# Kernel optimization log

Measured on AMD Instinct MI355X. Metric: run time of the kernel, lower is better.

## Reference

```python
import jax, jax.numpy as jnp
import numpy as np

COUPLE_STRENGTH = 0.1
ITER_FISTA = 16
ITER_EIGENVAL = 20


def setup_inputs() -> dict:
    key = jax.random.key(0)
    k1, k2 = jax.random.split(key)
    # light field patches: (b, N, u, v, s, t, ch)
    x = jax.random.normal(k1, (8, 256, 5, 5, 4, 4, 3), dtype=jnp.float32)
    dim_signal = 5 * 5 * 4 * 4 * 3  # 1200
    dim_dict = 2 * dim_signal       # overcompleteness = 2 -> 2400
    D = jax.random.normal(k2, (dim_signal, dim_dict), dtype=jnp.float32)
    D = D / jnp.linalg.norm(D, axis=0, keepdims=True)  # UnitNorm(axis=0) constraint
    return {"x": x, "dictionary": D}


def _max_eigval(D):
    """von Mises power iteration for largest eigenvalue of D^T D."""
    v0 = jax.random.normal(jax.random.key(42), (D.shape[1],), dtype=D.dtype)
    v0 = v0 / jnp.linalg.norm(v0)

    def step(v, _):
        w = D.T @ (D @ v)
        n = jnp.linalg.norm(w)
        return w / n, n

    _, norms = jax.lax.scan(step, v0, None, length=ITER_EIGENVAL)
    return norms[-1]


def _soft_threshold(x, thr):
    return jnp.sign(x) * jnp.maximum(jnp.abs(x) - thr, 0.0)


def _sparse_code_fista(x2, D):
    """x2: (B, N, dim_signal); D: (dim_signal, dim_dict) -> codes (B, N, dim_dict)."""
    L = _max_eigval(D)            # Lipschitz constant of grad of 0.5*||Dz - x||^2
    thr = COUPLE_STRENGTH / L
    z0 = jnp.zeros(x2.shape[:-1] + (D.shape[1],), dtype=x2.dtype)
    carry0 = (z0, z0, jnp.float32(1.0))  # (z, y, t)

    def step(carry, _):
        z, y, t = carry
        recon = jnp.einsum('bnk,dk->bnd', y, D)             # (B,N,ds)
        grad = jnp.einsum('bnd,dk->bnk', recon - x2, D)     # (B,N,dd)
        z_new = _soft_threshold(y - grad / L, thr)
        t_new = 0.5 * (1.0 + jnp.sqrt(1.0 + 4.0 * t * t))
        y_new = z_new + ((t - 1.0) / t_new) * (z_new - z)   # Nesterov momentum
        return (z_new, y_new, t_new), None

    (z, _, _), _ = jax.lax.scan(step, carry0, None, length=ITER_FISTA)
    return z


def reference(x, dictionary):
    B, N, u, v, s, t, ch = x.shape
    x2 = x.reshape(B, N, u * v * s * t * ch)
    code = jax.lax.stop_gradient(_sparse_code_fista(x2, dictionary))
    recon = jnp.einsum('bnk,dk->bnd', code, dictionary)  # matmul(x, D, transpose_b=True)
    return recon.reshape(B, N, u, v, s, t, ch)
```

## Files before the change

### kernel.cpp

```cpp
#include <hip/hip_runtime.h>
#include <hip/hip_bf16.h>
#include <cmath>

#define DS 1200
#define DD 2400
#define MR 2048
#define KP 1216
#define NP1 1280
#define NG 2432
#define PPI 150

typedef __attribute__((ext_vector_type(8))) short s16x8;
typedef __attribute__((ext_vector_type(4))) float f32x4;

__device__ __forceinline__ float s2f(short s) {
    union { unsigned u; float f; } c;
    c.u = ((unsigned)(unsigned short)s) << 16;
    return c.f;
}
__device__ __forceinline__ short f2s(float f) {
    __hip_bfloat16 h = __float2bfloat16(f);
    return *reinterpret_cast<short*>(&h);
}


__device__ __forceinline__ unsigned rotl32(unsigned x, int d) {
    return (x << d) | (x >> (32 - d));
}

__device__ void threefry2x32(unsigned k0, unsigned k1, unsigned x0, unsigned x1,
                             unsigned* o0, unsigned* o1) {
    unsigned ks0 = k0, ks1 = k1, ks2 = k0 ^ k1 ^ 0x1BD11BDAu;
    const int rotA[4] = {13, 15, 26, 6};
    const int rotB[4] = {17, 29, 16, 24};
    x0 += ks0; x1 += ks1;
    #pragma unroll
    for (int r = 0; r < 4; r++) { x0 += x1; x1 = rotl32(x1, rotA[r]); x1 ^= x0; }
    x0 += ks1; x1 += ks2 + 1u;
    #pragma unroll
    for (int r = 0; r < 4; r++) { x0 += x1; x1 = rotl32(x1, rotB[r]); x1 ^= x0; }
    x0 += ks2; x1 += ks0 + 2u;
    #pragma unroll
    for (int r = 0; r < 4; r++) { x0 += x1; x1 = rotl32(x1, rotA[r]); x1 ^= x0; }
    x0 += ks0; x1 += ks1 + 3u;
    #pragma unroll
    for (int r = 0; r < 4; r++) { x0 += x1; x1 = rotl32(x1, rotB[r]); x1 ^= x0; }
    x0 += ks1; x1 += ks2 + 4u;
    #pragma unroll
    for (int r = 0; r < 4; r++) { x0 += x1; x1 = rotl32(x1, rotA[r]); x1 ^= x0; }
    x0 += ks2; x1 += ks0 + 5u;
    *o0 = x0; *o1 = x1;
}

__device__ float erfinv_f32(float x) {
    float w = -logf((1.0f - x) * (1.0f + x));
    float p;
    if (w < 5.0f) {
        w -= 2.5f;
        p = 2.81022636e-08f;
        p = fmaf(p, w, 3.43273939e-07f);
        p = fmaf(p, w, -3.5233877e-06f);
        p = fmaf(p, w, -4.39150654e-06f);
        p = fmaf(p, w, 0.00021858087f);
        p = fmaf(p, w, -0.00125372503f);
        p = fmaf(p, w, -0.00417768164f);
        p = fmaf(p, w, 0.246640727f);
        p = fmaf(p, w, 1.50140941f);
    } else {
        w = sqrtf(w) - 3.0f;
        p = -0.000200214257f;
        p = fmaf(p, w, 0.000100950558f);
        p = fmaf(p, w, 0.00134934322f);
        p = fmaf(p, w, -0.00367342844f);
        p = fmaf(p, w, 0.00573950773f);
        p = fmaf(p, w, -0.0076224613f);
        p = fmaf(p, w, 0.00943887047f);
        p = fmaf(p, w, 1.00167406f);
        p = fmaf(p, w, 2.83297682f);
    }
    return p * x;
}

__device__ float bits_to_normal(unsigned bits) {
    unsigned fb = (bits >> 9) | 0x3F800000u;
    float u01 = __uint_as_float(fb) - 1.0f;
    const float lo = -0.99999994f;
    float u = u01 * 2.0f + lo;
    u = fmaxf(lo, u);
    return 1.41421356237f * erfinv_f32(u);
}

__global__ void k_init(float* __restrict__ w0, float* __restrict__ w1,
                       float* __restrict__ part) {
    int tid = threadIdx.x;
    for (int i = tid; i < 21 * PPI; i += 256) part[i] = 0.0f;
    if (tid < 32) {
        w0[2400 + tid] = 0.0f;
        w1[2400 + tid] = 0.0f;
    }
    __shared__ float red[256];
    float local2 = 0.0f;
    for (int p = tid; p < DS; p += 256) {
        unsigned r0, r1;
        threefry2x32(0u, 42u, (unsigned)p, (unsigned)(DS + p), &r0, &r1);
        float n0 = bits_to_normal(r0);
        float n1 = bits_to_normal(r1);
        w0[p] = n0;
        w0[DS + p] = n1;
        local2 += n0 * n0 + n1 * n1;
    }
    red[tid] = local2;
    __syncthreads();
    for (int s = 128; s > 0; s >>= 1) {
        if (tid < s) red[tid] += red[tid + s];
        __syncthreads();
    }
    if (tid == 0) part[0] = red[0];
}

__global__ __launch_bounds__(1024) void k_gmv(const short* __restrict__ Grm,
                                              const float* __restrict__ win,
                                              const float* __restrict__ partin,
                                              float* __restrict__ wout,
                                              float* __restrict__ partout) {
    float s2 = 0.0f;
    for (int i = 0; i < PPI; i++) s2 += partin[i];
    float rn = 1.0f / sqrtf(s2);
    int wave = threadIdx.x >> 6, lane = threadIdx.x & 63;
    int row = blockIdx.x * 16 + wave;
    const s16x8* gh = (const s16x8*)(Grm + (size_t)row * NG);
    const float4* w4 = (const float4*)win;
    float acc = 0.0f;
    #pragma unroll
    for (int i = 0; i < 5; i++) {
        int c = lane + i * 64;
        if (c < 304) {
            s16x8 h = gh[c];
            float4 wa = w4[c * 2], wb = w4[c * 2 + 1];
            acc += s2f(h[0]) * wa.x + s2f(h[1]) * wa.y;
            acc += s2f(h[2]) * wa.z + s2f(h[3]) * wa.w;
            acc += s2f(h[4]) * wb.x + s2f(h[5]) * wb.y;
            acc += s2f(h[6]) * wb.z + s2f(h[7]) * wb.w;
        }
    }
    #pragma unroll
    for (int off = 32; off > 0; off >>= 1) acc += __shfl_xor(acc, off, 64);
    __shared__ float red[16];
    if (lane == 0) {
        float val = acc * rn;
        wout[row] = val;
        red[wave] = val * val;
    }
    __syncthreads();
    if (threadIdx.x == 0) {
        float s = 0.0f;
        #pragma unroll
        for (int i = 0; i < 16; i++) s += red[i];
        partout[blockIdx.x] = s;
    }
}

__global__ void k_fin(const float* __restrict__ part20, float* __restrict__ scal) {
    if (threadIdx.x == 0) {
        float s = 0.0f;
        for (int i = 0; i < PPI; i++) s += part20[i];
        float L = sqrtf(s);
        scal[0] = L;
        scal[1] = 1.0f / L;
        scal[2] = 0.1f / L;
    }
}

__global__ void k_makeD(const float* __restrict__ D, short* __restrict__ Dp) {
    int p = blockIdx.x * 256 + threadIdx.x;
    if (p >= NP1 * NG) return;
    int tile = p >> 10, win = p & 1023;
    int row = win >> 3, e = win & 7;
    int mt = tile / (NG >> 3), ct = tile % (NG >> 3);
    int d = mt * 128 + row, n = ct * 8 + e;
    float v = (d < DS && n < DD) ? D[(size_t)d * DD + n] : 0.0f;
    Dp[p] = f2s(v);
}

__global__ void k_makeX(const float* __restrict__ x,
                        short* __restrict__ Xhi, short* __restrict__ Xlo) {
    int p = blockIdx.x * 256 + threadIdx.x;
    if (p >= MR * KP) return;
    int tile = p >> 10, win = p & 1023;
    int row = win >> 3, e = win & 7;
    int mt = tile / (KP >> 3), ct = tile % (KP >> 3);
    int m = mt * 128 + row, k = ct * 8 + e;
    float v = (k < DS) ? x[(size_t)m * DS + k] : 0.0f;
    short h = f2s(v);
    Xhi[p] = h;
    Xlo[p] = f2s(v - s2f(h));
}

__global__ void k_makeDt(const float* __restrict__ D,
                         short* __restrict__ Dthi, short* __restrict__ Dtlo) {
    __shared__ float t[32][33];
    int bc = blockIdx.x * 32;
    int bk = blockIdx.y * 32;
    int tx = threadIdx.x & 31, ty = threadIdx.x >> 5;
    for (int i = ty; i < 32; i += 8) {
        int k = bk + i, c = bc + tx;
        t[i][tx] = (k < DS && c < DD) ? D[(size_t)k * DD + c] : 0.0f;
    }
    __syncthreads();
    for (int i = ty; i < 32; i += 8) {
        int c = bc + i, k = bk + tx;
        float v = t[tx][i];
        short h = f2s(v);
        size_t po = ((size_t)(c >> 7) * (KP >> 3) + (k >> 3)) * 1024 +
                    ((c & 127) << 3) + (k & 7);
        Dthi[po] = h;
        Dtlo[po] = f2s(v - s2f(h));
    }
}

__global__ void k_fista0(const float* __restrict__ XD, const float* __restrict__ scal,
                         short* __restrict__ Z, short* __restrict__ Y) {
    int i = blockIdx.x * 256 + threadIdx.x;
    if (i >= MR * NG / 8) return;
    float invL = scal[1], thr = scal[2];
    int e0 = i * 8;
    int band = e0 / (128 * NG);
    int rem = e0 - band * (128 * NG);
    int tile = rem >> 10;
    int row = (rem & 1023) >> 3;
    int m = band * 128 + row;
    int n = tile * 8;
    const float4* xp = (const float4*)(XD + (size_t)m * NG + n);
    float4 v0 = xp[0], v1 = xp[1];
    float vs[8] = {v0.x, v0.y, v0.z, v0.w, v1.x, v1.y, v1.z, v1.w};
    s16x8 zs;
    #pragma unroll
    for (int k = 0; k < 8; k++) {
        float gs = vs[k] * invL;
        float az = fabsf(gs) - thr;
        float zn = (az > 0.0f) ? copysignf(az, gs) : 0.0f;
        zs[k] = f2s(zn);
    }
    ((s16x8*)Z)[i] = zs;
    ((s16x8*)Y)[i] = zs;
}

__device__ __forceinline__ void gload16(const void* g, void* l) {
    __builtin_amdgcn_global_load_lds(
        (const __attribute__((address_space(1))) unsigned int*)g,
        (__attribute__((address_space(3))) unsigned int*)l, 16, 0, 0);
}

template <int EPI, bool SPLIT>
__global__ __launch_bounds__(256, 4) void mfma_gemm(
    const short* __restrict__ Ah, const short* __restrict__ Al, int CA,
    const short* __restrict__ Bh, const short* __restrict__ Bl, int CB,
    int K, int swz,
    const float* __restrict__ XDc, const float* __restrict__ scal, float mom,
    short* __restrict__ Ynew, short* __restrict__ Zst,
    short* __restrict__ Gp, short* __restrict__ Grm,
    float* __restrict__ Out) {
    constexpr int ALO = 2048;
    constexpr int BHO = SPLIT ? 4096 : 2048;
    constexpr int BLO = 8192;
    constexpr int BUF = SPLIT ? 12288 : 6144;
    __shared__ __align__(16) short lds[2 * BUF];

    const int tid = threadIdx.x;
    const int w = tid >> 6, lane = tid & 63;
    const int fm = lane & 15, kg = lane >> 4;
    const int wr = w >> 1, wc = w & 1;

    int bx, by;
    if (swz) {
        int q = gridDim.x >> 3;
        int s = (blockIdx.x & 7) * q + (blockIdx.x >> 3);
        by = s & 31; bx = s >> 5;
    } else { bx = blockIdx.x; by = blockIdx.y; }
    const int m0 = by * 64, n0 = bx * 128;

    f32x4 acc[2][4];
    #pragma unroll
    for (int g = 0; g < 2; ++g)
        #pragma unroll
        for (int h = 0; h < 4; ++h) acc[g][h] = f32x4{0.f, 0.f, 0.f, 0.f};

    float invL = 0.0f, thr = 0.0f;
    if (EPI == 2) { invL = scal[1]; thr = scal[2]; }

    const int half = (m0 >> 6) & 1;
    const size_t Aoff = (size_t)(m0 & ~127) * CA + w * 1024 + half * 512 + lane * 8;
    const size_t Boff = (size_t)n0 * CB + w * 512 + lane * 8;

    const int nk = K >> 5;

    auto STAGE = [&](int t, int cur) {
        const int kk = t << 12;
        short* bp = &lds[cur * BUF];
        gload16(Ah + Aoff + kk, bp + w * 512);
        gload16(Bh + Boff + kk, bp + BHO + w * 512);
        gload16(Bh + Boff + kk + 2048, bp + BHO + 2048 + w * 512);
        if constexpr (SPLIT) {
            gload16(Al + Aoff + kk, bp + ALO + w * 512);
            gload16(Bl + Boff + kk, bp + BLO + w * 512);
            gload16(Bl + Boff + kk + 2048, bp + BLO + 2048 + w * 512);
        }
    };

    STAGE(0, 0);

    for (int t = 0; t < nk; ++t) {
        __syncthreads();
        if (t + 1 < nk) STAGE(t + 1, (t + 1) & 1);
        const short* bs = &lds[(t & 1) * BUF];

        s16x8 a[2], b[4];
        #pragma unroll
        for (int g = 0; g < 2; ++g)
            a[g] = *(const s16x8*)&bs[kg * 512 + (wr * 32 + g * 16 + fm) * 8];
        #pragma unroll
        for (int h = 0; h < 4; ++h)
            b[h] = *(const s16x8*)&bs[BHO + kg * 1024 + (wc * 64 + h * 16 + fm) * 8];
        if constexpr (SPLIT) {
            s16x8 a2[2], b2[4];
            #pragma unroll
            for (int g = 0; g < 2; ++g)
                a2[g] = *(const s16x8*)&bs[ALO + kg * 512 + (wr * 32 + g * 16 + fm) * 8];
            #pragma unroll
            for (int h = 0; h < 4; ++h)
                b2[h] = *(const s16x8*)&bs[BLO + kg * 1024 + (wc * 64 + h * 16 + fm) * 8];
            #pragma unroll
            for (int g = 0; g < 2; ++g)
                #pragma unroll
                for (int h = 0; h < 4; ++h) {
                    acc[g][h] = __builtin_amdgcn_mfma_f32_16x16x32_bf16(a[g], b[h], acc[g][h], 0, 0, 0);
                    acc[g][h] = __builtin_amdgcn_mfma_f32_16x16x32_bf16(a[g], b2[h], acc[g][h], 0, 0, 0);
                    acc[g][h] = __builtin_amdgcn_mfma_f32_16x16x32_bf16(a2[g], b[h], acc[g][h], 0, 0, 0);
                }
        } else {
            #pragma unroll
            for (int g = 0; g < 2; ++g)
                #pragma unroll
                for (int h = 0; h < 4; ++h)
                    acc[g][h] = __builtin_amdgcn_mfma_f32_16x16x32_bf16(a[g], b[h], acc[g][h], 0, 0, 0);
        }
    }

    #pragma unroll
    for (int g = 0; g < 2; ++g) {
        #pragma unroll
        for (int h = 0; h < 4; ++h) {
            #pragma unroll
            for (int j = 0; j < 4; ++j) {
                int m = m0 + wr * 32 + g * 16 + kg * 4 + j;
                int n = n0 + wc * 64 + h * 16 + fm;
                float v = acc[g][h][j];
                if (EPI == 0) {
                    if (n < DS) Out[(size_t)m * DS + n] = v;
                } else if (EPI == 2) {
                    size_t o = (size_t)m * NG + n;
                    size_t pz = (size_t)(m & ~127) * NG + ((n >> 3) << 10) +
                                ((m & 127) << 3) + (n & 7);
                    float grad = v - XDc[o];
                    float yold = s2f(Ah[pz]);
                    float zold = s2f(Zst[pz]);
                    float gs = yold - grad * invL;
                    float az = fabsf(gs) - thr;
                    float zn = (az > 0.0f) ? copysignf(az, gs) : 0.0f;
                    float yn = zn + mom * (zn - zold);
                    Zst[pz] = f2s(zn);
                    Ynew[pz] = f2s(yn);
                } else if (EPI == 3) {
                    Out[(size_t)m * NG + n] = v;
                } else {
                    size_t pz = (size_t)(m & ~127) * NG + ((n >> 3) << 10) +
                                ((m & 127) << 3) + (n & 7);
                    short hv = f2s(v);
                    Gp[pz] = hv;
                    Grm[(size_t)m * NG + n] = hv;
                }
            }
        }
    }
}

extern "C" void kernel_launch(void* const* d_in, const int* in_sizes, int n_in,
                              void* d_out, int out_size, void* d_ws, size_t ws_size,
                              hipStream_t stream) {
    const float* x = (const float*)d_in[0];
    const float* D = (const float*)d_in[1];
    float* out = (float*)d_out;

    char* wsb = (char*)d_ws;
    float* w0 = (float*)wsb;
    float* w1 = w0 + 2432;
    float* part = w1 + 2432;
    float* scal = part + 3200;

    char* p = wsb + 65536;
    short* Dp   = (short*)p; p += (size_t)NP1 * NG * 2;
    short* Dthi = (short*)p; p += (size_t)NG * KP * 2;
    short* Dtlo = (short*)p; p += (size_t)NG * KP * 2;
    short* Xhi  = (short*)p; p += (size_t)MR * KP * 2;
    short* Xlo  = (short*)p; p += (size_t)MR * KP * 2;
    short* Gp   = (short*)p; p += (size_t)NG * NG * 2;
    short* Grm  = (short*)p; p += (size_t)NG * NG * 2;
    float* XD   = (float*)p; p += (size_t)MR * NG * 4;
    short* Ya   = (short*)p; p += (size_t)MR * NG * 2;
    short* Yb   = (short*)p; p += (size_t)MR * NG * 2;
    short* Zp   = (short*)p; p += (size_t)MR * NG * 2;

    k_makeD<<<(NP1 * NG + 255) / 256, 256, 0, stream>>>(D, Dp);
    k_makeDt<<<dim3(NG / 32, KP / 32), 256, 0, stream>>>(D, Dthi, Dtlo);
    k_makeX<<<(MR * KP + 255) / 256, 256, 0, stream>>>(x, Xhi, Xlo);

    mfma_gemm<4, true><<<dim3(NG / 128, NG / 64), 256, 0, stream>>>(
        Dthi, Dtlo, KP, Dthi, Dtlo, KP, KP, 0,
        nullptr, nullptr, 0.0f, nullptr, nullptr, Gp, Grm, nullptr);

    mfma_gemm<3, true><<<dim3(608), 256, 0, stream>>>(
        Xhi, Xlo, KP, Dthi, Dtlo, KP, KP, 1,
        nullptr, nullptr, 0.0f, nullptr, nullptr, nullptr, nullptr, XD);

    k_init<<<1, 256, 0, stream>>>(w0, w1, part);
    for (int j = 0; j < 20; j++) {
        const float* win = (j & 1) ? w1 : w0;
        float* wout = (j & 1) ? w0 : w1;
        k_gmv<<<PPI, 1024, 0, stream>>>(Grm, win, part + j * PPI, wout,
                                        part + (j + 1) * PPI);
    }
    k_fin<<<1, 64, 0, stream>>>(part + 20 * PPI, scal);

    k_fista0<<<(MR * NG / 8 + 255) / 256, 256, 0, stream>>>(XD, scal, Zp, Ya);

    float t = 1.6180339887f;
    for (int i = 1; i < 16; i++) {
        float tn = 0.5f * (1.0f + sqrtf(1.0f + 4.0f * t * t));
        float mom = (t - 1.0f) / tn;
        t = tn;
        short* Yc = (i & 1) ? Ya : Yb;
        short* Yn = (i & 1) ? Yb : Ya;
        mfma_gemm<2, false><<<dim3(608), 256, 0, stream>>>(
            Yc, nullptr, NG, Gp, nullptr, NG, NG, 1,
            XD, scal, mom, Yn, Zp, nullptr, nullptr, nullptr);
    }

    mfma_gemm<0, false><<<dim3(320), 256, 0, stream>>>(
        Zp, nullptr, NG, Dp, nullptr, NG, NG, 1,
        nullptr, nullptr, 0.0f, nullptr, nullptr, nullptr, nullptr, out);
}
```

Measured before the change: 940.5 us.

## Fold identity and step size into Gram matrix; deepen K per stage in FISTA GEMM

Builds W = I - G/L in bf16 once after the power iteration, so each FISTA step computes y·W directly and the epilogue becomes a single fma with XD·invL instead of reading the old Y and subtracting. The non-split GEMM path now stages 64-wide K slices per barrier, two MFMA sub-steps per stage, halving the number of syncs and loop iterations. It adds an fp32 Gram buffer (aliased onto Ya) and a conversion kernel, and puts the identity-plus-scaled-Gram values into bf16, which may change rounding.

```diff
diff --git a/kernel.cpp b/kernel.cpp
--- a/kernel.cpp
+++ b/kernel.cpp
@@ -218,6 +218,30 @@
     }
 }
 
+__global__ void k_makeW(const float* __restrict__ Gf, const float* __restrict__ scal,
+                        short* __restrict__ Wp) {
+    int i = blockIdx.x * 256 + threadIdx.x;
+    if (i >= NG * NG / 8) return;
+    float invL = scal[1];
+    int e0 = i * 8;
+    int band = e0 / (128 * NG);
+    int rem = e0 - band * (128 * NG);
+    int tile = rem >> 10;
+    int row = (rem & 1023) >> 3;
+    int m = band * 128 + row;
+    int k0 = tile * 8;
+    const float4* gp = (const float4*)(Gf + (size_t)m * NG + k0);
+    float4 g0 = gp[0], g1 = gp[1];
+    float gv[8] = {g0.x, g0.y, g0.z, g0.w, g1.x, g1.y, g1.z, g1.w};
+    s16x8 wv;
+    #pragma unroll
+    for (int e = 0; e < 8; e++) {
+        float wf = ((k0 + e == m) ? 1.0f : 0.0f) - gv[e] * invL;
+        wv[e] = f2s(wf);
+    }
+    ((s16x8*)Wp)[i] = wv;
+}
+
 __global__ void k_fista0(const float* __restrict__ XD, const float* __restrict__ scal,
                          short* __restrict__ Z, short* __restrict__ Y) {
     int i = blockIdx.x * 256 + threadIdx.x;
@@ -258,12 +282,12 @@
     int K, int swz,
     const float* __restrict__ XDc, const float* __restrict__ scal, float mom,
     short* __restrict__ Ynew, short* __restrict__ Zst,
-    short* __restrict__ Gp, short* __restrict__ Grm,
+    short* __restrict__ Grm,
     float* __restrict__ Out) {
     constexpr int ALO = 2048;
-    constexpr int BHO = SPLIT ? 4096 : 2048;
+    constexpr int BHO = 4096;
     constexpr int BLO = 8192;
-    constexpr int BUF = SPLIT ? 12288 : 6144;
+    constexpr int BUF = 12288;
     __shared__ __align__(16) short lds[2 * BUF];
 
     const int tid = threadIdx.x;
@@ -289,21 +313,32 @@
     if (EPI == 2) { invL = scal[1]; thr = scal[2]; }
 
     const int half = (m0 >> 6) & 1;
-    const size_t Aoff = (size_t)(m0 & ~127) * CA + w * 1024 + half * 512 + lane * 8;
-    const size_t Boff = (size_t)n0 * CB + w * 512 + lane * 8;
-
-    const int nk = K >> 5;
+    const int nk = K / (SPLIT ? 32 : 64);
+
+    const size_t AbS = (size_t)(m0 & ~127) * CA + w * 1024 + half * 512 + lane * 8;
+    const size_t BbS = (size_t)n0 * CB + w * 512 + lane * 8;
+    const size_t AbN = (size_t)(m0 & ~127) * CA + half * 512 + lane * 8;
+    const size_t BbN = (size_t)n0 * CB + lane * 8;
 
     auto STAGE = [&](int t, int cur) {
-        const int kk = t << 12;
         short* bp = &lds[cur * BUF];
-        gload16(Ah + Aoff + kk, bp + w * 512);
-        gload16(Bh + Boff + kk, bp + BHO + w * 512);
-        gload16(Bh + Boff + kk + 2048, bp + BHO + 2048 + w * 512);
         if constexpr (SPLIT) {
-            gload16(Al + Aoff + kk, bp + ALO + w * 512);
-            gload16(Bl + Boff + kk, bp + BLO + w * 512);
-            gload16(Bl + Boff + kk + 2048, bp + BLO + 2048 + w * 512);
+            const size_t kk = (size_t)t << 12;
+            gload16(Ah + AbS + kk, bp + w * 512);
+            gload16(Bh + BbS + kk, bp + BHO + w * 512);
+            gload16(Bh + BbS + kk + 2048, bp + BHO + 2048 + w * 512);
+            gload16(Al + AbS + kk, bp + ALO + w * 512);
+            gload16(Bl + BbS + kk, bp + BLO + w * 512);
+            gload16(Bl + BbS + kk + 2048, bp + BLO + 2048 + w * 512);
+        } else {
+            const size_t kk = (size_t)t << 13;
+            const int cs0 = 2 * w, cs1 = 2 * w + 1;
+            gload16(Ah + AbN + kk + cs0 * 1024, bp + cs0 * 512);
+            gload16(Ah + AbN + kk + cs1 * 1024, bp + cs1 * 512);
+            gload16(Bh + BbN + kk + cs0 * 1024,       bp + BHO + cs0 * 1024);
+            gload16(Bh + BbN + kk + cs0 * 1024 + 512, bp + BHO + cs0 * 1024 + 512);
+            gload16(Bh + BbN + kk + cs1 * 1024,       bp + BHO + cs1 * 1024);
+            gload16(Bh + BbN + kk + cs1 * 1024 + 512, bp + BHO + cs1 * 1024 + 512);
         }
     };
 
@@ -314,35 +349,39 @@
         if (t + 1 < nk) STAGE(t + 1, (t + 1) & 1);
         const short* bs = &lds[(t & 1) * BUF];
 
-        s16x8 a[2], b[4];
         #pragma unroll
-        for (int g = 0; g < 2; ++g)
-            a[g] = *(const s16x8*)&bs[kg * 512 + (wr * 32 + g * 16 + fm) * 8];
-        #pragma unroll
-        for (int h = 0; h < 4; ++h)
-            b[h] = *(const s16x8*)&bs[BHO + kg * 1024 + (wc * 64 + h * 16 + fm) * 8];
-        if constexpr (SPLIT) {
-            s16x8 a2[2], b2[4];
+        for (int ks = 0; ks < (SPLIT ? 1 : 2); ++ks) {
+            const int c = ks * 4 + kg;
+            s16x8 a[2], b[4];
             #pragma unroll
             for (int g = 0; g < 2; ++g)
-                a2[g] = *(const s16x8*)&bs[ALO + kg * 512 + (wr * 32 + g * 16 + fm) * 8];
+                a[g] = *(const s16x8*)&bs[c * 512 + (wr * 32 + g * 16 + fm) * 8];
             #pragma unroll
             for (int h = 0; h < 4; ++h)
-                b2[h] = *(const s16x8*)&bs[BLO + kg * 1024 + (wc * 64 + h * 16 + fm) * 8];
-            #pragma unroll
-            for (int g = 0; g < 2; ++g)
+                b[h] = *(const s16x8*)&bs[BHO + c * 1024 + (wc * 64 + h * 16 + fm) * 8];
+            if constexpr (SPLIT) {
+                s16x8 a2[2], b2[4];
                 #pragma unroll
-                for (int h = 0; h < 4; ++h) {
-                    acc[g][h] = __builtin_amdgcn_mfma_f32_16x16x32_bf16(a[g], b[h], acc[g][h], 0, 0, 0);
-                    acc[g][h] = __builtin_amdgcn_mfma_f32_16x16x32_bf16(a[g], b2[h], acc[g][h], 0, 0, 0);
-                    acc[g][h] = __builtin_amdgcn_mfma_f32_16x16x32_bf16(a2[g], b[h], acc[g][h], 0, 0, 0);
-                }
-        } else {
-            #pragma unroll
-            for (int g = 0; g < 2; ++g)
+                for (int g = 0; g < 2; ++g)
+                    a2[g] = *(const s16x8*)&bs[ALO + c * 512 + (wr * 32 + g * 16 + fm) * 8];
                 #pragma unroll
                 for (int h = 0; h < 4; ++h)
-                    acc[g][h] = __builtin_amdgcn_mfma_f32_16x16x32_bf16(a[g], b[h], acc[g][h], 0, 0, 0);
+                    b2[h] = *(const s16x8*)&bs[BLO + c * 1024 + (wc * 64 + h * 16 + fm) * 8];
+                #pragma unroll
+                for (int g = 0; g < 2; ++g)
+                    #pragma unroll
+                    for (int h = 0; h < 4; ++h) {
+                        acc[g][h] = __builtin_amdgcn_mfma_f32_16x16x32_bf16(a[g], b[h], acc[g][h], 0, 0, 0);
+                        acc[g][h] = __builtin_amdgcn_mfma_f32_16x16x32_bf16(a[g], b2[h], acc[g][h], 0, 0, 0);
+                        acc[g][h] = __builtin_amdgcn_mfma_f32_16x16x32_bf16(a2[g], b[h], acc[g][h], 0, 0, 0);
+                    }
+            } else {
+                #pragma unroll
+                for (int g = 0; g < 2; ++g)
+                    #pragma unroll
+                    for (int h = 0; h < 4; ++h)
+                        acc[g][h] = __builtin_amdgcn_mfma_f32_16x16x32_bf16(a[g], b[h], acc[g][h], 0, 0, 0);
+            }
         }
     }
 
@@ -361,23 +400,19 @@
                     size_t o = (size_t)m * NG + n;
                     size_t pz = (size_t)(m & ~127) * NG + ((n >> 3) << 10) +
                                 ((m & 127) << 3) + (n & 7);
-                    float grad = v - XDc[o];
-                    float yold = s2f(Ah[pz]);
-                    float zold = s2f(Zst[pz]);
-                    float gs = yold - grad * invL;
+                    float gs = fmaf(XDc[o], invL, v);
                     float az = fabsf(gs) - thr;
                     float zn = (az > 0.0f) ? copysignf(az, gs) : 0.0f;
+                    float zold = s2f(Zst[pz]);
                     float yn = zn + mom * (zn - zold);
                     Zst[pz] = f2s(zn);
                     Ynew[pz] = f2s(yn);
                 } else if (EPI == 3) {
                     Out[(size_t)m * NG + n] = v;
                 } else {
-                    size_t pz = (size_t)(m & ~127) * NG + ((n >> 3) << 10) +
-                                ((m & 127) << 3) + (n & 7);
-                    short hv = f2s(v);
-                    Gp[pz] = hv;
-                    Grm[(size_t)m * NG + n] = hv;
+                    size_t o = (size_t)m * NG + n;
+                    Grm[o] = f2s(v);
+                    Out[o] = v;
                 }
             }
         }
@@ -403,12 +438,13 @@
     short* Dtlo = (short*)p; p += (size_t)NG * KP * 2;
     short* Xhi  = (short*)p; p += (size_t)MR * KP * 2;
     short* Xlo  = (short*)p; p += (size_t)MR * KP * 2;
-    short* Gp   = (short*)p; p += (size_t)NG * NG * 2;
+    short* Wp   = (short*)p; p += (size_t)NG * NG * 2;
     short* Grm  = (short*)p; p += (size_t)NG * NG * 2;
     float* XD   = (float*)p; p += (size_t)MR * NG * 4;
     short* Ya   = (short*)p; p += (size_t)MR * NG * 2;
     short* Yb   = (short*)p; p += (size_t)MR * NG * 2;
     short* Zp   = (short*)p; p += (size_t)MR * NG * 2;
+    float* Gf   = (float*)Ya;
 
     k_makeD<<<(NP1 * NG + 255) / 256, 256, 0, stream>>>(D, Dp);
     k_makeDt<<<dim3(NG / 32, KP / 32), 256, 0, stream>>>(D, Dthi, Dtlo);
@@ -416,11 +452,7 @@
 
     mfma_gemm<4, true><<<dim3(NG / 128, NG / 64), 256, 0, stream>>>(
         Dthi, Dtlo, KP, Dthi, Dtlo, KP, KP, 0,
-        nullptr, nullptr, 0.0f, nullptr, nullptr, Gp, Grm, nullptr);
-
-    mfma_gemm<3, true><<<dim3(608), 256, 0, stream>>>(
-        Xhi, Xlo, KP, Dthi, Dtlo, KP, KP, 1,
-        nullptr, nullptr, 0.0f, nullptr, nullptr, nullptr, nullptr, XD);
+        nullptr, nullptr, 0.0f, nullptr, nullptr, Grm, Gf);
 
     k_init<<<1, 256, 0, stream>>>(w0, w1, part);
     for (int j = 0; j < 20; j++) {
@@ -430,6 +462,12 @@
                                         part + (j + 1) * PPI);
     }
     k_fin<<<1, 64, 0, stream>>>(part + 20 * PPI, scal);
+
+    k_makeW<<<(NG * NG / 8 + 255) / 256, 256, 0, stream>>>(Gf, scal, Wp);
+
+    mfma_gemm<3, true><<<dim3(608), 256, 0, stream>>>(
+        Xhi, Xlo, KP, Dthi, Dtlo, KP, KP, 1,
+        nullptr, nullptr, 0.0f, nullptr, nullptr, nullptr, XD);
 
     k_fista0<<<(MR * NG / 8 + 255) / 256, 256, 0, stream>>>(XD, scal, Zp, Ya);
 
@@ -441,11 +479,11 @@
         short* Yc = (i & 1) ? Ya : Yb;
         short* Yn = (i & 1) ? Yb : Ya;
         mfma_gemm<2, false><<<dim3(608), 256, 0, stream>>>(
-            Yc, nullptr, NG, Gp, nullptr, NG, NG, 1,
-            XD, scal, mom, Yn, Zp, nullptr, nullptr, nullptr);
+            Yc, nullptr, NG, Wp, nullptr, NG, NG, 1,
+            XD, scal, mom, Yn, Zp, nullptr, nullptr);
     }
 
     mfma_gemm<0, false><<<dim3(320), 256, 0, stream>>>(
         Zp, nullptr, NG, Dp, nullptr, NG, NG, 1,
-        nullptr, nullptr, 0.0f, nullptr, nullptr, nullptr, nullptr, out);
-}
+        nullptr, nullptr, 0.0f, nullptr, nullptr, nullptr, out);
+}
```

After: 882.3 us. 6.2% less time.
